# Kernel tuning notes

Measured on AMD Instinct MI355X. Metric: run time of the kernel, lower is better.

The kernel has to match this reference:

```python
import jax, jax.numpy as jnp
import numpy as np
from jax.ops import segment_sum, segment_max

N = 20000   # nodes
E = 320000  # edges (no self loops; conv adds them)
G = 64      # graphs in batch
D = 128     # embed dim
H = 64      # GATConv out channels (heads=1)
L = 6       # number of conv/mlp blocks


def setup_inputs() -> dict:
    key = jax.random.key(0)
    ks = jax.random.split(key, 24)
    x_idx = jax.random.randint(ks[0], (N,), 0, 128)
    src = jax.random.randint(ks[1], (E,), 0, N)
    dst = jax.random.randint(ks[2], (E,), 0, N)
    dst = jnp.where(src == dst, (dst + 1) % N, dst)  # remove_self_loops semantics
    edge_index = jnp.stack([src, dst])
    edge_attr_idx = jax.random.randint(ks[3], (E,), 0, 128)
    batch = (jnp.arange(N) * G) // N  # sorted graph ids, ~312 nodes/graph
    s = 0.1
    r = lambda k, shp: jax.random.normal(k, shp, dtype=jnp.float32) * s
    return {
        'x_idx': x_idx, 'edge_index': edge_index, 'edge_attr_idx': edge_attr_idx, 'batch': batch,
        'emb': r(ks[4], (128, D)),
        'conv_W': r(ks[5], (L, D, H)), 'conv_We': r(ks[6], (L, D, H)),
        'conv_att_src': r(ks[7], (L, H)), 'conv_att_dst': r(ks[8], (L, H)),
        'conv_att_edge': r(ks[9], (L, H)), 'conv_b': jnp.zeros((L, H), jnp.float32),
        'mlp_W1': r(ks[10], (L, H, H)), 'mlp_b1': jnp.zeros((L, H), jnp.float32),
        'mlp_W2': r(ks[11], (L, H, H)), 'mlp_b2': jnp.zeros((L, H), jnp.float32),
        'mlp_W3': r(ks[12], (L, H, D)), 'mlp_b3': jnp.zeros((L, D), jnp.float32),
        'g1_W1': r(ks[13], (D, H)), 'g1_b1': jnp.zeros((H,), jnp.float32),
        'g1_W2': r(ks[14], (H, 1)), 'g1_b2': jnp.zeros((1,), jnp.float32),
        'g2_W1': r(ks[15], (D, H)), 'g2_b1': jnp.zeros((H,), jnp.float32),
        'g2_W2': r(ks[16], (H, D)), 'g2_b2': jnp.zeros((D,), jnp.float32),
        'p_W1': r(ks[17], (D, H)), 'p_b1': jnp.zeros((H,), jnp.float32),
        'p_W2': r(ks[18], (H, H)), 'p_b2': jnp.zeros((H,), jnp.float32),
        'p_W3': r(ks[19], (H, 1)), 'p_b3': jnp.zeros((1,), jnp.float32),
    }


def _mlp3(x, W1, b1, W2, b2, W3, b3):
    h = jax.nn.relu(x @ W1 + b1)
    h = jax.nn.relu(h @ W2 + b2)
    return h @ W3 + b3


def reference(x_idx, edge_index, edge_attr_idx, batch, emb, conv_W, conv_We,
              conv_att_src, conv_att_dst, conv_att_edge, conv_b,
              mlp_W1, mlp_b1, mlp_W2, mlp_b2, mlp_W3, mlp_b3,
              g1_W1, g1_b1, g1_W2, g1_b2, g2_W1, g2_b1, g2_W2, g2_b2,
              p_W1, p_b1, p_W2, p_b2, p_W3, p_b3):
    n = x_idx.shape[0]
    x = emb[x_idx]                 # [N,128]
    e = emb[edge_attr_idx]         # [E,128]
    src, dst = edge_index[0], edge_index[1]
    # add_self_loops with fill_value='mean': loop attr = mean of incoming edge attrs
    deg = segment_sum(jnp.ones((e.shape[0],), x.dtype), dst, num_segments=n)
    loop_attr = segment_sum(e, dst, num_segments=n) / jnp.maximum(deg, 1.0)[:, None]
    e_full = jnp.concatenate([e, loop_attr], axis=0)             # [E+N,128]
    ar = jnp.arange(n)
    src_f = jnp.concatenate([src, ar])
    dst_f = jnp.concatenate([dst, ar])

    def gat_conv(x, i):
        h = x @ conv_W[i]                       # [N,64]
        ep = e_full @ conv_We[i]                # [E+N,64]
        a_s = h @ conv_att_src[i]               # [N]
        a_d = h @ conv_att_dst[i]               # [N]
        a_e = ep @ conv_att_edge[i]             # [E+N]
        logit = jax.nn.leaky_relu(a_s[src_f] + a_d[dst_f] + a_e, 0.2)
        m = segment_max(logit, dst_f, num_segments=n)
        w = jnp.exp(logit - m[dst_f])
        denom = segment_sum(w, dst_f, num_segments=n)
        alpha = w / denom[dst_f]
        out = segment_sum(h[src_f] * alpha[:, None], dst_f, num_segments=n)
        return out + conv_b[i]

    jkn = []
    for i in range(L):  # dropout is identity at inference
        x = gat_conv(x, i)
        x = _mlp3(x, mlp_W1[i], mlp_b1[i], mlp_W2[i], mlp_b2[i], mlp_W3[i], mlp_b3[i])
        jkn.append(x)
    jkn = jnp.stack(jkn)                                  # [6,N,128]
    ms = jnp.sqrt(jnp.sum(jnp.square(jkn), axis=2))       # [6,N]
    ni = jnp.argmax(ms, axis=0)                           # [N]
    feature = jnp.take_along_axis(jkn, ni[None, :, None], axis=0)[0]  # [N,128]

    # per-graph attention pooling (vectorized over the per-graph loop)
    h1 = (jax.nn.relu(feature @ g1_W1 + g1_b1) @ g1_W2 + g1_b2)[:, 0]  # [N]
    m = segment_max(h1, batch, num_segments=G)
    w = jnp.exp(h1 - m[batch])
    attn = w / segment_sum(w, batch, num_segments=G)[batch]            # softmax per graph
    h2 = jax.nn.relu(feature @ g2_W1 + g2_b1) @ g2_W2 + g2_b2          # [N,128]
    counts = segment_sum(jnp.ones((n,), feature.dtype), batch, num_segments=G)
    hg = segment_sum(attn[:, None] * h2, batch, num_segments=G) / counts[:, None]  # [G,128]

    out = _mlp3(hg, p_W1, p_b1, p_W2, p_b2, p_W3, p_b3)   # [G,1]
    return out[:, 0]
```

## Files before the change

### kernel.cpp

```cpp
#include <hip/hip_runtime.h>
#include <math.h>

__device__ __forceinline__ float lrelu(float x){ return x > 0.0f ? x : 0.2f*x; }
__device__ __forceinline__ float bcastf(float v, int l){
    return __int_as_float(__builtin_amdgcn_readlane(__float_as_int(v), l));
}


__global__ void k_count(const int* __restrict__ dst, int* __restrict__ cnt, int E){
    int e = blockIdx.x*256 + threadIdx.x;
    if(e < E) atomicAdd(&cnt[dst[e]], 1);
}

__global__ __launch_bounds__(1024) void k_scan(const int* __restrict__ cnt, int* __restrict__ rowptr, int n){
    __shared__ int ws[16];
    __shared__ int carrysh;
    int t = threadIdx.x, lane = t & 63, wv = t >> 6;
    if(t==0){ carrysh = 0; rowptr[0] = 0; }
    __syncthreads();
    for(int base=0; base<n; base+=1024){
        int i = base + t;
        int v = (i<n) ? cnt[i] : 0;
        int s = v;
        #pragma unroll
        for(int off=1; off<64; off<<=1){ int u = __shfl_up(s, off, 64); if(lane>=off) s += u; }
        if(lane==63) ws[wv] = s;
        __syncthreads();
        if(t < 16){
            int u = ws[t];
            #pragma unroll
            for(int off=1; off<16; off<<=1){ int u2 = __shfl_up(u, off, 16); if(t>=off) u += u2; }
            ws[t] = u;
        }
        __syncthreads();
        int carry = carrysh;
        int wbase = wv ? ws[wv-1] : 0;
        if(i<n) rowptr[i+1] = carry + wbase + s;
        int total = ws[15];
        __syncthreads();
        if(t==0) carrysh = carry + total;
        __syncthreads();
    }
}

__global__ void k_scatter(const int* __restrict__ dst, const int* __restrict__ rowptr,
                          int* __restrict__ cnt2, int* __restrict__ eid, int E){
    int e = blockIdx.x*256 + threadIdx.x;
    if(e >= E) return;
    int d = dst[e];
    int p = rowptr[d] + atomicAdd(&cnt2[d], 1);
    eid[p] = e;
}

__global__ __launch_bounds__(256) void k_sortb(const int* __restrict__ rowptr, int* __restrict__ eid, int n){
    int node = blockIdx.x*4 + (threadIdx.x>>6);
    if(node >= n) return;
    int lane = threadIdx.x & 63;
    int b = rowptr[node], e = rowptr[node+1];
    int nj = e - b;
    if(nj <= 1) return;
    if(nj <= 64){
        int v = (lane < nj) ? eid[b+lane] : 0x7fffffff;
        for(int k=2; k<=64; k<<=1){
            for(int j=k>>1; j>0; j>>=1){
                int vv = __shfl_xor(v, j, 64);
                bool up = ((lane & k) == 0);
                bool lower = ((lane & j) == 0);
                int mn = min(v,vv), mx = max(v,vv);
                v = (lower == up) ? mn : mx;
            }
        }
        if(lane < nj) eid[b+lane] = v;
    } else if(lane == 0){
        for(int i=b+1; i<e; i++){
            int key = eid[i]; int j = i-1;
            while(j>=b && eid[j] > key){ eid[j+1] = eid[j]; j--; }
            eid[j+1] = key;
        }
    }
}

__global__ __launch_bounds__(768) void k_table(const float* __restrict__ We, const float* __restrict__ atte,
                                               const float* __restrict__ emb, float* __restrict__ T){
    __shared__ float wv[768];
    int t = threadIdx.x;
    {
        int l = t>>7, k = t&127;
        const float* w = We + ((size_t)l*128 + k)*64;
        const float* a = atte + l*64;
        float s = 0.f;
        #pragma unroll 8
        for(int c=0;c<64;c++) s += w[c]*a[c];
        wv[t] = s;
    }
    __syncthreads();
    int l = t>>7, a = t&127;
    const float4* er = (const float4*)(emb + (size_t)a*128);
    const float* w = wv + l*128;
    float acc = 0.f;
    for(int k=0;k<32;k++){
        float4 v = er[k];
        acc += v.x*w[k*4+0] + v.y*w[k*4+1] + v.z*w[k*4+2] + v.w*w[k*4+3];
    }
    T[l*128 + a] = acc;
}

__global__ __launch_bounds__(256) void k_ae2(const int* __restrict__ eid, const int* __restrict__ src,
                     const int* __restrict__ eattr, const float* __restrict__ T,
                     int* __restrict__ csrsrc, float* __restrict__ ae, int E){
    __shared__ float Tl[768];
    for(int i=threadIdx.x; i<768; i+=256) Tl[i] = T[i];
    __syncthreads();
    int p = blockIdx.x*256 + threadIdx.x;
    if(p >= E) return;
    int e = eid[p];
    csrsrc[p] = src[e];
    int a = eattr[e];
    #pragma unroll
    for(int l=0;l<6;l++) ae[(size_t)l*E + p] = Tl[l*128 + a];
}


__global__ __launch_bounds__(512) void k_hx(const int* __restrict__ xidx, const float* __restrict__ emb,
        const float* __restrict__ W, const float* __restrict__ atts, const float* __restrict__ attd,
        float* __restrict__ h, float* __restrict__ as_, float* __restrict__ ad_, int n){
    __shared__ float xs[64][129];
    __shared__ float hs[64][65];
    __shared__ float redA[8][64], redB[8][64];
    int base = blockIdx.x*64;
    int t = threadIdx.x;
    {
        int r = t>>3, c0 = (t&7)*16;
        if(base + r < n){
            const float4* srcp = (const float4*)(emb + (size_t)xidx[base+r]*128 + c0);
            #pragma unroll
            for(int q=0;q<4;q++){
                float4 v = srcp[q];
                xs[r][c0+q*4+0]=v.x; xs[r][c0+q*4+1]=v.y; xs[r][c0+q*4+2]=v.z; xs[r][c0+q*4+3]=v.w;
            }
        } else {
            #pragma unroll
            for(int q=0;q<16;q++) xs[r][c0+q] = 0.f;
        }
    }
    __syncthreads();
    int lane = t & 63;
    int wid = __builtin_amdgcn_readfirstlane(t >> 6);
    int cb = wid*8;
    float acc[8] = {0,0,0,0,0,0,0,0};
    for(int k=0;k<128;k++){
        float xv = xs[lane][k];
        #pragma unroll
        for(int cc=0;cc<8;cc++) acc[cc] = fmaf(xv, W[k*64 + cb + cc], acc[cc]);
    }
    float pa=0.f, pd=0.f;
    #pragma unroll
    for(int cc=0;cc<8;cc++){
        hs[lane][cb+cc] = acc[cc];
        pa += acc[cc]*atts[cb+cc];
        pd += acc[cc]*attd[cb+cc];
    }
    redA[wid][lane]=pa; redB[wid][lane]=pd;
    __syncthreads();
    {
        int r = t>>3, c0 = (t&7)*8;
        if(base + r < n){
            float* dst = h + (size_t)(base+r)*64 + c0;
            #pragma unroll
            for(int q=0;q<8;q++) dst[q] = hs[r][c0+q];
        }
    }
    if(t < 64 && base + t < n){
        float sa=0.f, sd=0.f;
        #pragma unroll
        for(int w=0;w<8;w++){ sa += redA[w][t]; sd += redB[w][t]; }
        as_[base+t] = sa; ad_[base+t] = sd;
    }
}


__global__ __launch_bounds__(256) void k_gat(const float* __restrict__ h,
        const float* __restrict__ as_, const float* __restrict__ ad_,
        const float* __restrict__ ae, const int* __restrict__ rowptr,
        const int* __restrict__ csrsrc, const float* __restrict__ bias,
        float* __restrict__ o, int n){
    int node = blockIdx.x*4 + (threadIdx.x>>6);
    if(node >= n) return;
    int lane = threadIdx.x & 63;
    int b = rowptr[node], e = rowptr[node+1];
    float adv = ad_[node];
    float m = -1e30f, d = 0.f, sumae = 0.f;
    float a0=0.f, a1=0.f, a2=0.f, a3=0.f;
    for(int j0=b; j0<e; j0+=64){
        int nj = min(64, e-j0);
        int sj = 0; float aev = 0.f, lg = -1e30f;
        if(lane < nj){
            sj  = csrsrc[j0+lane];
            aev = ae[j0+lane];
            lg  = lrelu(as_[sj] + adv + aev);
        }
        float cm = lg, sa = aev;
        #pragma unroll
        for(int off=32; off; off>>=1){ cm = fmaxf(cm, __shfl_xor(cm,off,64)); sa += __shfl_xor(sa,off,64); }
        sumae += sa;
        float nm = fmaxf(m, cm);
        float w = (lane<nj) ? expf(lg-nm) : 0.f;
        float ws = w;
        #pragma unroll
        for(int off=32; off; off>>=1) ws += __shfl_xor(ws,off,64);
        float scale = (m > -1e29f) ? expf(m-nm) : 0.f;
        d = d*scale + ws;
        a0*=scale; a1*=scale; a2*=scale; a3*=scale;
        int j = 0;
        for(; j+3<nj; j+=4){
            a0 = fmaf(bcastf(w,j+0), h[(size_t)__builtin_amdgcn_readlane(sj,j+0)*64 + lane], a0);
            a1 = fmaf(bcastf(w,j+1), h[(size_t)__builtin_amdgcn_readlane(sj,j+1)*64 + lane], a1);
            a2 = fmaf(bcastf(w,j+2), h[(size_t)__builtin_amdgcn_readlane(sj,j+2)*64 + lane], a2);
            a3 = fmaf(bcastf(w,j+3), h[(size_t)__builtin_amdgcn_readlane(sj,j+3)*64 + lane], a3);
        }
        for(; j<nj; j++)
            a0 = fmaf(bcastf(w,j), h[(size_t)__builtin_amdgcn_readlane(sj,j)*64 + lane], a0);
        m = nm;
    }
    int deg = e - b;
    float ael = sumae / fmaxf((float)deg, 1.f);
    float ls = lrelu(as_[node] + adv + ael);
    float nm = fmaxf(m, ls);
    float scale = (m > -1e29f) ? expf(m-nm) : 0.f;
    float wl = expf(ls-nm);
    d = d*scale + wl;
    float acc = (a0+a1)+(a2+a3);
    acc = acc*scale + wl*h[(size_t)node*64 + lane];
    o[(size_t)node*64 + lane] = acc/d + bias[lane];
}


__global__ __launch_bounds__(512) void k_dense(
    const float* __restrict__ o,
    const float* __restrict__ W1, const float* __restrict__ b1,
    const float* __restrict__ W2, const float* __restrict__ b2,
    const float* __restrict__ W3, const float* __restrict__ b3,
    float* __restrict__ bestF, float* __restrict__ bestMs, int layer,
    const float* __restrict__ Wn, const float* __restrict__ atts, const float* __restrict__ attd,
    float* __restrict__ hn, float* __restrict__ asn, float* __restrict__ adn_,
    const float* __restrict__ A, const float* __restrict__ g1b1,
    const float* __restrict__ w2, const float* __restrict__ g1b2,
    const float* __restrict__ B, const float* __restrict__ g2b1,
    const float* __restrict__ C, const float* __restrict__ g2b2,
    float* __restrict__ h1, float* __restrict__ h2,
    int n, int last)
{
    __shared__ float o_s[64][65];
    __shared__ float xs[64][129];
    __shared__ float redA[8][64], redB[8][64];
    __shared__ unsigned char updf[64];
    int base = blockIdx.x*64;
    int t = threadIdx.x, lane = t & 63;
    int wid = __builtin_amdgcn_readfirstlane(t >> 6);

    {
        int r = t>>3, c0 = (t&7)*8;
        if(base + r < n){
            const float4* srcp = (const float4*)(o + (size_t)(base+r)*64 + c0);
            float4 v0 = srcp[0], v1 = srcp[1];
            o_s[r][c0+0]=v0.x; o_s[r][c0+1]=v0.y; o_s[r][c0+2]=v0.z; o_s[r][c0+3]=v0.w;
            o_s[r][c0+4]=v1.x; o_s[r][c0+5]=v1.y; o_s[r][c0+6]=v1.z; o_s[r][c0+7]=v1.w;
        } else {
            #pragma unroll
            for(int q=0;q<8;q++) o_s[r][c0+q] = 0.f;
        }
    }
    __syncthreads();

    {
        int cb = wid*8;
        float acc[8];
        #pragma unroll
        for(int cc=0;cc<8;cc++) acc[cc] = b1[cb+cc];
        for(int k=0;k<64;k++){
            float ov = o_s[lane][k];
            #pragma unroll
            for(int cc=0;cc<8;cc++) acc[cc] = fmaf(ov, W1[k*64 + cb + cc], acc[cc]);
        }
        #pragma unroll
        for(int cc=0;cc<8;cc++) xs[lane][cb+cc] = fmaxf(acc[cc], 0.f);
    }
    __syncthreads();

    {
        int cb = wid*8;
        float acc[8];
        #pragma unroll
        for(int cc=0;cc<8;cc++) acc[cc] = b2[cb+cc];
        for(int k=0;k<64;k++){
            float tv = xs[lane][k];
            #pragma unroll
            for(int cc=0;cc<8;cc++) acc[cc] = fmaf(tv, W2[k*64 + cb + cc], acc[cc]);
        }
        __syncthreads();
        #pragma unroll
        for(int cc=0;cc<8;cc++) o_s[lane][cb+cc] = fmaxf(acc[cc], 0.f);
    }
    __syncthreads();

    {
        int cb = wid*16;
        float acc[16];
        #pragma unroll
        for(int cc=0;cc<16;cc++) acc[cc] = b3[cb+cc];
        for(int k=0;k<64;k++){
            float tv = o_s[lane][k];
            #pragma unroll
            for(int cc=0;cc<16;cc++) acc[cc] = fmaf(tv, W3[k*128 + cb + cc], acc[cc]);
        }
        float ms = 0.f;
        #pragma unroll
        for(int cc=0;cc<16;cc++){ xs[lane][cb+cc] = acc[cc]; ms += acc[cc]*acc[cc]; }
        redA[wid][lane] = ms;
    }
    __syncthreads();

    if(t < 64){
        int node = base + t; bool u = false;
        if(node < n){
            float ms = 0.f;
            #pragma unroll
            for(int w=0;w<8;w++) ms += redA[w][t];
            u = (layer==0) || (ms > bestMs[node]);
            if(u) bestMs[node] = ms;
        }
        updf[t] = u ? 1 : 0;
    }
    __syncthreads();

    if(!last){
        {
            int r = t>>3, c0 = (t&7)*16;
            if(updf[r] && base + r < n){
                float* dst = bestF + (size_t)(base+r)*128 + c0;
                #pragma unroll
                for(int q=0;q<16;q++) dst[q] = xs[r][c0+q];
            }
        }
        {
            int cb = wid*8;
            float acc[8] = {0,0,0,0,0,0,0,0};
            for(int k=0;k<128;k++){
                float xv = xs[lane][k];
                #pragma unroll
                for(int cc=0;cc<8;cc++) acc[cc] = fmaf(xv, Wn[k*64 + cb + cc], acc[cc]);
            }
            float pa=0.f, pd=0.f;
            #pragma unroll
            for(int cc=0;cc<8;cc++){
                o_s[lane][cb+cc] = acc[cc];
                pa += acc[cc]*atts[cb+cc];
                pd += acc[cc]*attd[cb+cc];
            }
            redA[wid][lane]=pa; redB[wid][lane]=pd;
        }
        __syncthreads();
        {
            int r = t>>3, c0 = (t&7)*8;
            if(base + r < n){
                float* dst = hn + (size_t)(base+r)*64 + c0;
                #pragma unroll
                for(int q=0;q<8;q++) dst[q] = o_s[r][c0+q];
            }
        }
        if(t < 64 && base + t < n){
            float sa=0.f, sd=0.f;
            #pragma unroll
            for(int w=0;w<8;w++){ sa += redA[w][t]; sd += redB[w][t]; }
            asn[base+t] = sa; adn_[base+t] = sd;
        }
        return;
    }

    {
        int r = t>>3, c0 = (t&7)*16;
        if(!updf[r] && base + r < n){
            const float4* srcp = (const float4*)(bestF + (size_t)(base+r)*128 + c0);
            #pragma unroll
            for(int q=0;q<4;q++){
                float4 v = srcp[q];
                xs[r][c0+q*4+0]=v.x; xs[r][c0+q*4+1]=v.y; xs[r][c0+q*4+2]=v.z; xs[r][c0+q*4+3]=v.w;
            }
        }
    }
    __syncthreads();
    if(wid < 4){
        int cb = wid*16;
        float acc[16];
        #pragma unroll
        for(int cc=0;cc<16;cc++) acc[cc] = g1b1[cb+cc];
        for(int k=0;k<128;k++){
            float fv = xs[lane][k];
            #pragma unroll
            for(int cc=0;cc<16;cc++) acc[cc] = fmaf(fv, A[k*64 + cb + cc], acc[cc]);
        }
        float pp = 0.f;
        #pragma unroll
        for(int cc=0;cc<16;cc++) pp += fmaxf(acc[cc],0.f)*w2[cb+cc];
        redA[wid][lane] = pp;
    } else {
        int cb = (wid-4)*16;
        float acc[16];
        #pragma unroll
        for(int cc=0;cc<16;cc++) acc[cc] = g2b1[cb+cc];
        for(int k=0;k<128;k++){
            float fv = xs[lane][k];
            #pragma unroll
            for(int cc=0;cc<16;cc++) acc[cc] = fmaf(fv, B[k*64 + cb + cc], acc[cc]);
        }
        #pragma unroll
        for(int cc=0;cc<16;cc++) o_s[lane][cb+cc] = fmaxf(acc[cc],0.f);
    }
    __syncthreads();
    if(t < 64 && base + t < n)
        h1[base+t] = redA[0][t]+redA[1][t]+redA[2][t]+redA[3][t] + g1b2[0];
    {
        int cb = wid*16;
        float acc[16];
        #pragma unroll
        for(int cc=0;cc<16;cc++) acc[cc] = g2b2[cb+cc];
        for(int k=0;k<64;k++){
            float tv = o_s[lane][k];
            #pragma unroll
            for(int cc=0;cc<16;cc++) acc[cc] = fmaf(tv, C[k*128 + cb + cc], acc[cc]);
        }
        __syncthreads();
        #pragma unroll
        for(int cc=0;cc<16;cc++) xs[lane][cb+cc] = acc[cc];
    }
    __syncthreads();
    {
        int r = t>>3, c0 = (t&7)*16;
        if(base + r < n){
            float* dst = h2 + (size_t)(base+r)*128 + c0;
            #pragma unroll
            for(int q=0;q<16;q++) dst[q] = xs[r][c0+q];
        }
    }
}


__global__ __launch_bounds__(128) void k_pool2(const float* __restrict__ h1, const float* __restrict__ h2,
                      float* __restrict__ wbuf,
                      const float* __restrict__ pW1, const float* __restrict__ pb1,
                      const float* __restrict__ pW2, const float* __restrict__ pb2,
                      const float* __restrict__ pW3, const float* __restrict__ pb3,
                      float* __restrict__ out, int n, int G){
    __shared__ float sh[128];
    __shared__ float hgrow[128];
    int g = blockIdx.x, tid = threadIdx.x;
    int start = (g*n + G-1)/G, end = ((g+1)*n + G-1)/G;
    float lm = -1e30f;
    for(int i=start+tid; i<end; i+=128) lm = fmaxf(lm, h1[i]);
    sh[tid]=lm; __syncthreads();
    for(int off=64; off; off>>=1){ if(tid<off) sh[tid]=fmaxf(sh[tid],sh[tid+off]); __syncthreads(); }
    float m = sh[0]; __syncthreads();
    float lsum = 0.f;
    for(int i=start+tid; i<end; i+=128){ float w = expf(h1[i]-m); wbuf[i]=w; lsum+=w; }
    sh[tid]=lsum; __syncthreads();
    for(int off=64; off; off>>=1){ if(tid<off) sh[tid]+=sh[tid+off]; __syncthreads(); }
    float denom = sh[0];
    float a0=0.f,a1=0.f,a2=0.f,a3=0.f;
    int i = start;
    for(; i+3<end; i+=4){
        a0 = fmaf(wbuf[i+0], h2[(size_t)(i+0)*128 + tid], a0);
        a1 = fmaf(wbuf[i+1], h2[(size_t)(i+1)*128 + tid], a1);
        a2 = fmaf(wbuf[i+2], h2[(size_t)(i+2)*128 + tid], a2);
        a3 = fmaf(wbuf[i+3], h2[(size_t)(i+3)*128 + tid], a3);
    }
    for(; i<end; i++) a0 = fmaf(wbuf[i], h2[(size_t)i*128 + tid], a0);
    float acc = (a0+a1)+(a2+a3);
    hgrow[tid] = acc/denom/(float)(end-start);
    __syncthreads();
    if(tid < 64){
        float t1v = pb1[tid];
        for(int k=0;k<128;k++) t1v = fmaf(hgrow[k], pW1[k*64+tid], t1v);
        t1v = fmaxf(t1v, 0.f);
        float t2v = pb2[tid];
        for(int k=0;k<64;k++) t2v = fmaf(__shfl(t1v,k,64), pW2[k*64+tid], t2v);
        t2v = fmaxf(t2v, 0.f);
        float s = t2v * pW3[tid];
        #pragma unroll
        for(int off=32; off; off>>=1) s += __shfl_xor(s,off,64);
        if(tid==0) out[g] = s + pb3[0];
    }
}

extern "C" void kernel_launch(void* const* d_in, const int* in_sizes, int n_in,
                              void* d_out, int out_size, void* d_ws, size_t ws_size,
                              hipStream_t stream){
    const int*   x_idx   = (const int*)  d_in[0];
    const int*   eindex  = (const int*)  d_in[1];
    const int*   eattr   = (const int*)  d_in[2];
    const float* emb     = (const float*)d_in[4];
    const float* conv_W  = (const float*)d_in[5];
    const float* conv_We = (const float*)d_in[6];
    const float* att_src = (const float*)d_in[7];
    const float* att_dst = (const float*)d_in[8];
    const float* att_edg = (const float*)d_in[9];
    const float* conv_b  = (const float*)d_in[10];
    const float* mW1 = (const float*)d_in[11]; const float* mb1 = (const float*)d_in[12];
    const float* mW2 = (const float*)d_in[13]; const float* mb2 = (const float*)d_in[14];
    const float* mW3 = (const float*)d_in[15]; const float* mb3 = (const float*)d_in[16];
    const float* g1W1= (const float*)d_in[17]; const float* g1b1= (const float*)d_in[18];
    const float* g1W2= (const float*)d_in[19]; const float* g1b2= (const float*)d_in[20];
    const float* g2W1= (const float*)d_in[21]; const float* g2b1= (const float*)d_in[22];
    const float* g2W2= (const float*)d_in[23]; const float* g2b2= (const float*)d_in[24];
    const float* pW1 = (const float*)d_in[25]; const float* pb1 = (const float*)d_in[26];
    const float* pW2 = (const float*)d_in[27]; const float* pb2 = (const float*)d_in[28];
    const float* pW3 = (const float*)d_in[29]; const float* pb3 = (const float*)d_in[30];

    const int N = in_sizes[0];
    const int E = in_sizes[2];
    const int G = out_size;
    const int* src = eindex;
    const int* dst = eindex + E;
    const int NT = (N + 63) / 64;
    const int NW = (N + 3) / 4;

    char* p = (char*)d_ws;
    auto alloc = [&](size_t bytes)->void*{ void* r = (void*)p; p += (bytes + 255) & ~(size_t)255; return r; };
    float* h      = (float*)alloc((size_t)N*64*4);
    float* o      = (float*)alloc((size_t)N*64*4);
    float* bestF  = (float*)alloc((size_t)N*128*4);
    float* h2buf  = (float*)alloc((size_t)N*128*4);
    float* bestMs = (float*)alloc((size_t)N*4);
    float* as_    = (float*)alloc((size_t)N*4);
    float* ad_    = (float*)alloc((size_t)N*4);
    float* ae     = (float*)alloc((size_t)6*E*4);
    float* Tbuf   = (float*)alloc(6*128*4);
    float* h1     = (float*)alloc((size_t)N*4);
    int*   cnt    = (int*)  alloc((size_t)N*4);
    int*   cnt2   = (int*)  alloc((size_t)N*4);
    int*   rowptr = (int*)  alloc((size_t)(N+1)*4);
    int*   eid    = (int*)  alloc((size_t)E*4);
    int*   csrsrc = (int*)  alloc((size_t)E*4);

    hipMemsetAsync(cnt,  0, (size_t)N*4, stream);
    hipMemsetAsync(cnt2, 0, (size_t)N*4, stream);

    k_count<<<(E+255)/256, 256, 0, stream>>>(dst, cnt, E);
    k_scan<<<1, 1024, 0, stream>>>(cnt, rowptr, N);
    k_scatter<<<(E+255)/256, 256, 0, stream>>>(dst, rowptr, cnt2, eid, E);
    k_sortb<<<NW, 256, 0, stream>>>(rowptr, eid, N);
    k_table<<<1, 768, 0, stream>>>(conv_We, att_edg, emb, Tbuf);
    k_ae2<<<(E+255)/256, 256, 0, stream>>>(eid, src, eattr, Tbuf, csrsrc, ae, E);
    k_hx<<<NT, 512, 0, stream>>>(x_idx, emb, conv_W, att_src, att_dst, h, as_, ad_, N);

    for(int l=0; l<6; l++){
        int last = (l==5) ? 1 : 0;
        const float* Wn   = last ? conv_W  : conv_W  + (size_t)(l+1)*8192;
        const float* atsn = last ? att_src : att_src + (l+1)*64;
        const float* atdn = last ? att_dst : att_dst + (l+1)*64;
        k_gat<<<NW, 256, 0, stream>>>(h, as_, ad_, ae + (size_t)l*E, rowptr, csrsrc, conv_b + l*64, o, N);
        k_dense<<<NT, 512, 0, stream>>>(o,
            mW1 + (size_t)l*4096, mb1 + l*64, mW2 + (size_t)l*4096, mb2 + l*64,
            mW3 + (size_t)l*8192, mb3 + l*128,
            bestF, bestMs, l,
            Wn, atsn, atdn,
            h, as_, ad_,
            g1W1, g1b1, g1W2, g1b2, g2W1, g2b1, g2W2, g2b2,
            h1, h2buf,
            N, last);
    }

    k_pool2<<<G, 128, 0, stream>>>(h1, h2buf, bestMs,
            pW1, pb1, pW2, pb2, pW3, pb3, (float*)d_out, N, G);
}
```

Before: 446.6 us.

## Retile dense MLP kernel to 16 nodes per 256-thread block with float4 weights

The fused dense kernel changes from 64 nodes per 512-thread block, where each lane owned one node and one wave owned a column slice, to 16 nodes per 256-thread block. Each lane now owns one node and a group of 4 or 8 output columns, and weights are read as float4 vectors. This gives about four times as many blocks, which spreads the work across more CUs and cuts per-thread register pressure. In exchange, each block reloads every weight matrix for far fewer nodes, so weight traffic through L2 rises, and the reductions and g1/g2 branches are reorganised across 16 column groups.

```diff
diff --git a/kernel.cpp b/kernel.cpp
--- a/kernel.cpp
+++ b/kernel.cpp
@@ -235,7 +235,7 @@
 }
 
 
-__global__ __launch_bounds__(512) void k_dense(
+__global__ __launch_bounds__(256) void k_dense(
     const float* __restrict__ o,
     const float* __restrict__ W1, const float* __restrict__ b1,
     const float* __restrict__ W2, const float* __restrict__ b2,
@@ -250,84 +250,88 @@
     float* __restrict__ h1, float* __restrict__ h2,
     int n, int last)
 {
-    __shared__ float o_s[64][65];
-    __shared__ float xs[64][129];
-    __shared__ float redA[8][64], redB[8][64];
-    __shared__ unsigned char updf[64];
-    int base = blockIdx.x*64;
+    __shared__ float o_s[16][65];
+    __shared__ float xs[16][129];
+    __shared__ float redA[16][16], redB[16][16];
+    __shared__ unsigned char updf[16];
+    int base = blockIdx.x*16;
     int t = threadIdx.x, lane = t & 63;
     int wid = __builtin_amdgcn_readfirstlane(t >> 6);
-
-    {
-        int r = t>>3, c0 = (t&7)*8;
+    int node = lane & 15;
+    int q    = lane >> 4;
+    int grp  = wid*4 + q;
+    int cb4  = grp*4;
+    int cb8  = grp*8;
+
+    {
+        int r = t>>4, c0 = (t&15)*4;
         if(base + r < n){
-            const float4* srcp = (const float4*)(o + (size_t)(base+r)*64 + c0);
-            float4 v0 = srcp[0], v1 = srcp[1];
-            o_s[r][c0+0]=v0.x; o_s[r][c0+1]=v0.y; o_s[r][c0+2]=v0.z; o_s[r][c0+3]=v0.w;
-            o_s[r][c0+4]=v1.x; o_s[r][c0+5]=v1.y; o_s[r][c0+6]=v1.z; o_s[r][c0+7]=v1.w;
+            float4 v = *(const float4*)(o + (size_t)(base+r)*64 + c0);
+            o_s[r][c0+0]=v.x; o_s[r][c0+1]=v.y; o_s[r][c0+2]=v.z; o_s[r][c0+3]=v.w;
         } else {
-            #pragma unroll
-            for(int q=0;q<8;q++) o_s[r][c0+q] = 0.f;
-        }
-    }
-    __syncthreads();
-
-    {
-        int cb = wid*8;
+            o_s[r][c0+0]=0.f; o_s[r][c0+1]=0.f; o_s[r][c0+2]=0.f; o_s[r][c0+3]=0.f;
+        }
+    }
+    __syncthreads();
+
+    {
+        float acc[4];
+        #pragma unroll
+        for(int cc=0;cc<4;cc++) acc[cc] = b1[cb4+cc];
+        for(int k=0;k<64;k++){
+            float ov = o_s[node][k];
+            float4 w = *(const float4*)(W1 + k*64 + cb4);
+            acc[0]=fmaf(ov,w.x,acc[0]); acc[1]=fmaf(ov,w.y,acc[1]);
+            acc[2]=fmaf(ov,w.z,acc[2]); acc[3]=fmaf(ov,w.w,acc[3]);
+        }
+        #pragma unroll
+        for(int cc=0;cc<4;cc++) xs[node][cb4+cc] = fmaxf(acc[cc], 0.f);
+    }
+    __syncthreads();
+
+    {
+        float acc[4];
+        #pragma unroll
+        for(int cc=0;cc<4;cc++) acc[cc] = b2[cb4+cc];
+        for(int k=0;k<64;k++){
+            float tv = xs[node][k];
+            float4 w = *(const float4*)(W2 + k*64 + cb4);
+            acc[0]=fmaf(tv,w.x,acc[0]); acc[1]=fmaf(tv,w.y,acc[1]);
+            acc[2]=fmaf(tv,w.z,acc[2]); acc[3]=fmaf(tv,w.w,acc[3]);
+        }
+        #pragma unroll
+        for(int cc=0;cc<4;cc++) o_s[node][cb4+cc] = fmaxf(acc[cc], 0.f);
+    }
+    __syncthreads();
+
+    {
         float acc[8];
         #pragma unroll
-        for(int cc=0;cc<8;cc++) acc[cc] = b1[cb+cc];
+        for(int cc=0;cc<8;cc++) acc[cc] = b3[cb8+cc];
         for(int k=0;k<64;k++){
-            float ov = o_s[lane][k];
-            #pragma unroll
-            for(int cc=0;cc<8;cc++) acc[cc] = fmaf(ov, W1[k*64 + cb + cc], acc[cc]);
-        }
-        #pragma unroll
-        for(int cc=0;cc<8;cc++) xs[lane][cb+cc] = fmaxf(acc[cc], 0.f);
-    }
-    __syncthreads();
-
-    {
-        int cb = wid*8;
-        float acc[8];
-        #pragma unroll
-        for(int cc=0;cc<8;cc++) acc[cc] = b2[cb+cc];
-        for(int k=0;k<64;k++){
-            float tv = xs[lane][k];
-            #pragma unroll
-            for(int cc=0;cc<8;cc++) acc[cc] = fmaf(tv, W2[k*64 + cb + cc], acc[cc]);
-        }
-        __syncthreads();
-        #pragma unroll
-        for(int cc=0;cc<8;cc++) o_s[lane][cb+cc] = fmaxf(acc[cc], 0.f);
-    }
-    __syncthreads();
-
-    {
-        int cb = wid*16;
-        float acc[16];
-        #pragma unroll
-        for(int cc=0;cc<16;cc++) acc[cc] = b3[cb+cc];
-        for(int k=0;k<64;k++){
-            float tv = o_s[lane][k];
-            #pragma unroll
-            for(int cc=0;cc<16;cc++) acc[cc] = fmaf(tv, W3[k*128 + cb + cc], acc[cc]);
+            float tv = o_s[node][k];
+            float4 w0 = *(const float4*)(W3 + k*128 + cb8);
+            float4 w1 = *(const float4*)(W3 + k*128 + cb8 + 4);
+            acc[0]=fmaf(tv,w0.x,acc[0]); acc[1]=fmaf(tv,w0.y,acc[1]);
+            acc[2]=fmaf(tv,w0.z,acc[2]); acc[3]=fmaf(tv,w0.w,acc[3]);
+            acc[4]=fmaf(tv,w1.x,acc[4]); acc[5]=fmaf(tv,w1.y,acc[5]);
+            acc[6]=fmaf(tv,w1.z,acc[6]); acc[7]=fmaf(tv,w1.w,acc[7]);
         }
         float ms = 0.f;
         #pragma unroll
-        for(int cc=0;cc<16;cc++){ xs[lane][cb+cc] = acc[cc]; ms += acc[cc]*acc[cc]; }
-        redA[wid][lane] = ms;
-    }
-    __syncthreads();
-
-    if(t < 64){
-        int node = base + t; bool u = false;
-        if(node < n){
+        for(int cc=0;cc<8;cc++){ xs[node][cb8+cc] = acc[cc]; ms += acc[cc]*acc[cc]; }
+        redA[grp][node] = ms;
+    }
+    __syncthreads();
+
+    if(t < 16){
+        int nd = base + t; bool u = false;
+        if(nd < n){
             float ms = 0.f;
             #pragma unroll
-            for(int w=0;w<8;w++) ms += redA[w][t];
-            u = (layer==0) || (ms > bestMs[node]);
-            if(u) bestMs[node] = ms;
+            for(int g=0;g<16;g++) ms += redA[g][t];
+            u = (layer==0) || (ms > bestMs[nd]);
+            if(u) bestMs[nd] = ms;
         }
         updf[t] = u ? 1 : 0;
     }
@@ -335,111 +339,117 @@
 
     if(!last){
         {
-            int r = t>>3, c0 = (t&7)*16;
+            int r = t>>4, c0 = (t&15)*8;
             if(updf[r] && base + r < n){
                 float* dst = bestF + (size_t)(base+r)*128 + c0;
+                const float* s = &xs[r][c0];
                 #pragma unroll
-                for(int q=0;q<16;q++) dst[q] = xs[r][c0+q];
+                for(int qq=0;qq<8;qq++) dst[qq] = s[qq];
             }
         }
-        {
-            int cb = wid*8;
-            float acc[8] = {0,0,0,0,0,0,0,0};
-            for(int k=0;k<128;k++){
-                float xv = xs[lane][k];
-                #pragma unroll
-                for(int cc=0;cc<8;cc++) acc[cc] = fmaf(xv, Wn[k*64 + cb + cc], acc[cc]);
-            }
-            float pa=0.f, pd=0.f;
-            #pragma unroll
-            for(int cc=0;cc<8;cc++){
-                o_s[lane][cb+cc] = acc[cc];
-                pa += acc[cc]*atts[cb+cc];
-                pd += acc[cc]*attd[cb+cc];
-            }
-            redA[wid][lane]=pa; redB[wid][lane]=pd;
-        }
+        float acc[4] = {0,0,0,0};
+        for(int k=0;k<128;k++){
+            float xv = xs[node][k];
+            float4 w = *(const float4*)(Wn + k*64 + cb4);
+            acc[0]=fmaf(xv,w.x,acc[0]); acc[1]=fmaf(xv,w.y,acc[1]);
+            acc[2]=fmaf(xv,w.z,acc[2]); acc[3]=fmaf(xv,w.w,acc[3]);
+        }
+        float pa=0.f, pd=0.f;
+        #pragma unroll
+        for(int cc=0;cc<4;cc++){
+            pa += acc[cc]*atts[cb4+cc];
+            pd += acc[cc]*attd[cb4+cc];
+        }
+        redA[grp][node]=pa; redB[grp][node]=pd;
+        #pragma unroll
+        for(int cc=0;cc<4;cc++) o_s[node][cb4+cc] = acc[cc];
         __syncthreads();
         {
-            int r = t>>3, c0 = (t&7)*8;
+            int r = t>>4, c0 = (t&15)*4;
             if(base + r < n){
                 float* dst = hn + (size_t)(base+r)*64 + c0;
-                #pragma unroll
-                for(int q=0;q<8;q++) dst[q] = o_s[r][c0+q];
+                dst[0]=o_s[r][c0+0]; dst[1]=o_s[r][c0+1]; dst[2]=o_s[r][c0+2]; dst[3]=o_s[r][c0+3];
             }
         }
-        if(t < 64 && base + t < n){
+        if(t < 16 && base + t < n){
             float sa=0.f, sd=0.f;
             #pragma unroll
-            for(int w=0;w<8;w++){ sa += redA[w][t]; sd += redB[w][t]; }
+            for(int g=0;g<16;g++){ sa += redA[g][t]; sd += redB[g][t]; }
             asn[base+t] = sa; adn_[base+t] = sd;
         }
         return;
     }
 
     {
-        int r = t>>3, c0 = (t&7)*16;
+        int r = t>>4, c0 = (t&15)*8;
         if(!updf[r] && base + r < n){
-            const float4* srcp = (const float4*)(bestF + (size_t)(base+r)*128 + c0);
-            #pragma unroll
-            for(int q=0;q<4;q++){
-                float4 v = srcp[q];
-                xs[r][c0+q*4+0]=v.x; xs[r][c0+q*4+1]=v.y; xs[r][c0+q*4+2]=v.z; xs[r][c0+q*4+3]=v.w;
-            }
-        }
-    }
-    __syncthreads();
-    if(wid < 4){
-        int cb = wid*16;
-        float acc[16];
-        #pragma unroll
-        for(int cc=0;cc<16;cc++) acc[cc] = g1b1[cb+cc];
+            const float* s = bestF + (size_t)(base+r)*128 + c0;
+            float* d = &xs[r][c0];
+            #pragma unroll
+            for(int qq=0;qq<8;qq++) d[qq] = s[qq];
+        }
+    }
+    __syncthreads();
+    {
+        float acc[4];
+        #pragma unroll
+        for(int cc=0;cc<4;cc++) acc[cc] = g1b1[cb4+cc];
         for(int k=0;k<128;k++){
-            float fv = xs[lane][k];
-            #pragma unroll
-            for(int cc=0;cc<16;cc++) acc[cc] = fmaf(fv, A[k*64 + cb + cc], acc[cc]);
+            float fv = xs[node][k];
+            float4 w = *(const float4*)(A + k*64 + cb4);
+            acc[0]=fmaf(fv,w.x,acc[0]); acc[1]=fmaf(fv,w.y,acc[1]);
+            acc[2]=fmaf(fv,w.z,acc[2]); acc[3]=fmaf(fv,w.w,acc[3]);
         }
         float pp = 0.f;
         #pragma unroll
-        for(int cc=0;cc<16;cc++) pp += fmaxf(acc[cc],0.f)*w2[cb+cc];
-        redA[wid][lane] = pp;
-    } else {
-        int cb = (wid-4)*16;
-        float acc[16];
-        #pragma unroll
-        for(int cc=0;cc<16;cc++) acc[cc] = g2b1[cb+cc];
+        for(int cc=0;cc<4;cc++) pp += fmaxf(acc[cc],0.f)*w2[cb4+cc];
+        redA[grp][node] = pp;
+    }
+    {
+        float acc[4];
+        #pragma unroll
+        for(int cc=0;cc<4;cc++) acc[cc] = g2b1[cb4+cc];
         for(int k=0;k<128;k++){
-            float fv = xs[lane][k];
-            #pragma unroll
-            for(int cc=0;cc<16;cc++) acc[cc] = fmaf(fv, B[k*64 + cb + cc], acc[cc]);
-        }
-        #pragma unroll
-        for(int cc=0;cc<16;cc++) o_s[lane][cb+cc] = fmaxf(acc[cc],0.f);
-    }
-    __syncthreads();
-    if(t < 64 && base + t < n)
-        h1[base+t] = redA[0][t]+redA[1][t]+redA[2][t]+redA[3][t] + g1b2[0];
-    {
-        int cb = wid*16;
-        float acc[16];
-        #pragma unroll
-        for(int cc=0;cc<16;cc++) acc[cc] = g2b2[cb+cc];
+            float fv = xs[node][k];
+            float4 w = *(const float4*)(B + k*64 + cb4);
+            acc[0]=fmaf(fv,w.x,acc[0]); acc[1]=fmaf(fv,w.y,acc[1]);
+            acc[2]=fmaf(fv,w.z,acc[2]); acc[3]=fmaf(fv,w.w,acc[3]);
+        }
+        #pragma unroll
+        for(int cc=0;cc<4;cc++) o_s[node][cb4+cc] = fmaxf(acc[cc],0.f);
+    }
+    __syncthreads();
+    if(t < 16 && base + t < n){
+        float s = 0.f;
+        #pragma unroll
+        for(int g=0;g<16;g++) s += redA[g][t];
+        h1[base+t] = s + g1b2[0];
+    }
+    {
+        float acc[8];
+        #pragma unroll
+        for(int cc=0;cc<8;cc++) acc[cc] = g2b2[cb8+cc];
         for(int k=0;k<64;k++){
-            float tv = o_s[lane][k];
-            #pragma unroll
-            for(int cc=0;cc<16;cc++) acc[cc] = fmaf(tv, C[k*128 + cb + cc], acc[cc]);
+            float tv = o_s[node][k];
+            float4 w0 = *(const float4*)(C + k*128 + cb8);
+            float4 w1 = *(const float4*)(C + k*128 + cb8 + 4);
+            acc[0]=fmaf(tv,w0.x,acc[0]); acc[1]=fmaf(tv,w0.y,acc[1]);
+            acc[2]=fmaf(tv,w0.z,acc[2]); acc[3]=fmaf(tv,w0.w,acc[3]);
+            acc[4]=fmaf(tv,w1.x,acc[4]); acc[5]=fmaf(tv,w1.y,acc[5]);
+            acc[6]=fmaf(tv,w1.z,acc[6]); acc[7]=fmaf(tv,w1.w,acc[7]);
         }
         __syncthreads();
         #pragma unroll
-        for(int cc=0;cc<16;cc++) xs[lane][cb+cc] = acc[cc];
-    }
-    __syncthreads();
-    {
-        int r = t>>3, c0 = (t&7)*16;
+        for(int cc=0;cc<8;cc++) xs[node][cb8+cc] = acc[cc];
+    }
+    __syncthreads();
+    {
+        int r = t>>4, c0 = (t&15)*8;
         if(base + r < n){
             float* dst = h2 + (size_t)(base+r)*128 + c0;
-            #pragma unroll
-            for(int q=0;q<16;q++) dst[q] = xs[r][c0+q];
+            const float* s = &xs[r][c0];
+            #pragma unroll
+            for(int qq=0;qq<8;qq++) dst[qq] = s[qq];
         }
     }
 }
@@ -522,6 +532,7 @@
     const int* dst = eindex + E;
     const int NT = (N + 63) / 64;
     const int NW = (N + 3) / 4;
+    const int ND = (N + 15) / 16;
 
     char* p = (char*)d_ws;
     auto alloc = [&](size_t bytes)->void*{ void* r = (void*)p; p += (bytes + 255) & ~(size_t)255; return r; };
@@ -558,7 +569,7 @@
         const float* atsn = last ? att_src : att_src + (l+1)*64;
         const float* atdn = last ? att_dst : att_dst + (l+1)*64;
         k_gat<<<NW, 256, 0, stream>>>(h, as_, ad_, ae + (size_t)l*E, rowptr, csrsrc, conv_b + l*64, o, N);
-        k_dense<<<NT, 512, 0, stream>>>(o,
+        k_dense<<<ND, 256, 0, stream>>>(o,
             mW1 + (size_t)l*4096, mb1 + l*64, mW2 + (size_t)l*4096, mb2 + l*64,
             mW3 + (size_t)l*8192, mb3 + l*128,
             bestF, bestMs, l,
```

Result: slower. 643.3 us (+44.0%).

## Fold MLP output weights into next conv projection and precompute embedding projection

Applied to the files above, without the earlier changes.

Precomputes W3·W_next and b3·W_next per layer so the next-layer GAT projection runs as a 64-wide product on the MLP hidden state instead of a 128-wide one on the output. The first-layer projection and attention scalars are computed once per embedding vocabulary row and gathered per node. This cuts the per-node FMA work in the dense kernel and the initial projection, at the cost of a few small setup kernels and slight floating-point reassociation.

```diff
diff --git a/kernel.cpp b/kernel.cpp
--- a/kernel.cpp
+++ b/kernel.cpp
@@ -120,62 +120,74 @@
     for(int l=0;l<6;l++) ae[(size_t)l*E + p] = Tl[l*128 + a];
 }
 
-
-__global__ __launch_bounds__(512) void k_hx(const int* __restrict__ xidx, const float* __restrict__ emb,
-        const float* __restrict__ W, const float* __restrict__ atts, const float* __restrict__ attd,
-        float* __restrict__ h, float* __restrict__ as_, float* __restrict__ ad_, int n){
-    __shared__ float xs[64][129];
-    __shared__ float hs[64][65];
-    __shared__ float redA[8][64], redB[8][64];
-    int base = blockIdx.x*64;
+__global__ __launch_bounds__(256) void k_wcomb(const float* __restrict__ W3all, const float* __restrict__ Wnall,
+                                               const float* __restrict__ b3all,
+                                               float* __restrict__ Wcomb, float* __restrict__ bcomb){
+    int l = blockIdx.x;
+    const float* W3 = W3all + (size_t)l*8192;
+    const float* Wn = Wnall + (size_t)(l+1)*8192;
+    const float* b3 = b3all + l*128;
+    float* Wc = Wcomb + l*4096;
     int t = threadIdx.x;
-    {
-        int r = t>>3, c0 = (t&7)*16;
-        if(base + r < n){
-            const float4* srcp = (const float4*)(emb + (size_t)xidx[base+r]*128 + c0);
-            #pragma unroll
-            for(int q=0;q<4;q++){
-                float4 v = srcp[q];
-                xs[r][c0+q*4+0]=v.x; xs[r][c0+q*4+1]=v.y; xs[r][c0+q*4+2]=v.z; xs[r][c0+q*4+3]=v.w;
-            }
-        } else {
-            #pragma unroll
-            for(int q=0;q<16;q++) xs[r][c0+q] = 0.f;
-        }
-    }
-    __syncthreads();
-    int lane = t & 63;
-    int wid = __builtin_amdgcn_readfirstlane(t >> 6);
-    int cb = wid*8;
-    float acc[8] = {0,0,0,0,0,0,0,0};
+    for(int q=0;q<16;q++){
+        int o = t*16 + q;
+        int k = o>>6, c = o&63;
+        float s = 0.f;
+        for(int j=0;j<128;j++) s += W3[k*128+j]*Wn[j*64+c];
+        Wc[k*64+c] = s;
+    }
+    if(t < 64){
+        float s = 0.f;
+        for(int j=0;j<128;j++) s += b3[j]*Wn[j*64+t];
+        bcomb[l*64+t] = s;
+    }
+}
+
+__global__ __launch_bounds__(512) void k_hemb(const float* __restrict__ emb, const float* __restrict__ W0,
+                                              float* __restrict__ hemb){
+    int t = threadIdx.x;
+    int a = t>>2, c0 = (t&3)*16;
+    const float* er = emb + (size_t)a*128;
+    float acc[16];
+    #pragma unroll
+    for(int cc=0;cc<16;cc++) acc[cc] = 0.f;
     for(int k=0;k<128;k++){
-        float xv = xs[lane][k];
-        #pragma unroll
-        for(int cc=0;cc<8;cc++) acc[cc] = fmaf(xv, W[k*64 + cb + cc], acc[cc]);
-    }
-    float pa=0.f, pd=0.f;
+        float xv = er[k];
+        #pragma unroll
+        for(int cc=0;cc<16;cc++) acc[cc] = fmaf(xv, W0[k*64 + c0 + cc], acc[cc]);
+    }
     #pragma unroll
-    for(int cc=0;cc<8;cc++){
-        hs[lane][cb+cc] = acc[cc];
-        pa += acc[cc]*atts[cb+cc];
-        pd += acc[cc]*attd[cb+cc];
-    }
-    redA[wid][lane]=pa; redB[wid][lane]=pd;
-    __syncthreads();
-    {
-        int r = t>>3, c0 = (t&7)*8;
-        if(base + r < n){
-            float* dst = h + (size_t)(base+r)*64 + c0;
-            #pragma unroll
-            for(int q=0;q<8;q++) dst[q] = hs[r][c0+q];
-        }
-    }
-    if(t < 64 && base + t < n){
-        float sa=0.f, sd=0.f;
-        #pragma unroll
-        for(int w=0;w<8;w++){ sa += redA[w][t]; sd += redB[w][t]; }
-        as_[base+t] = sa; ad_[base+t] = sd;
-    }
+    for(int cc=0;cc<16;cc++) hemb[a*64 + c0 + cc] = acc[cc];
+}
+
+__global__ __launch_bounds__(128) void k_aemb(const float* __restrict__ hemb,
+                                              const float* __restrict__ atts, const float* __restrict__ attd,
+                                              float* __restrict__ aS, float* __restrict__ aD){
+    int a = threadIdx.x;
+    const float* hr = hemb + a*64;
+    float sa = 0.f, sd = 0.f;
+    for(int w=0;w<8;w++){
+        float pa = 0.f, pd = 0.f;
+        #pragma unroll
+        for(int cc=0;cc<8;cc++){
+            int c = w*8+cc;
+            pa += hr[c]*atts[c];
+            pd += hr[c]*attd[c];
+        }
+        sa += pa; sd += pd;
+    }
+    aS[a] = sa; aD[a] = sd;
+}
+
+__global__ void k_hx2(const int* __restrict__ xidx, const float* __restrict__ hemb,
+                      const float* __restrict__ aS, const float* __restrict__ aD,
+                      float* __restrict__ h, float* __restrict__ as_, float* __restrict__ ad_, int n){
+    int idx = blockIdx.x*256 + threadIdx.x;
+    if(idx >= n*16) return;
+    int node = idx>>4, q = idx&15, c0 = q*4;
+    int xi = xidx[node];
+    *(float4*)(h + (size_t)node*64 + c0) = *(const float4*)(hemb + (size_t)xi*64 + c0);
+    if(q==0){ as_[node] = aS[xi]; ad_[node] = aD[xi]; }
 }
 
 
@@ -241,7 +253,8 @@
     const float* __restrict__ W2, const float* __restrict__ b2,
     const float* __restrict__ W3, const float* __restrict__ b3,
     float* __restrict__ bestF, float* __restrict__ bestMs, int layer,
-    const float* __restrict__ Wn, const float* __restrict__ atts, const float* __restrict__ attd,
+    const float* __restrict__ Wc, const float* __restrict__ bc,
+    const float* __restrict__ atts, const float* __restrict__ attd,
     float* __restrict__ hn, float* __restrict__ asn, float* __restrict__ adn_,
     const float* __restrict__ A, const float* __restrict__ g1b1,
     const float* __restrict__ w2, const float* __restrict__ g1b2,
@@ -344,20 +357,24 @@
         }
         {
             int cb = wid*8;
-            float acc[8] = {0,0,0,0,0,0,0,0};
-            for(int k=0;k<128;k++){
-                float xv = xs[lane][k];
+            float acc[8];
+            #pragma unroll
+            for(int cc=0;cc<8;cc++) acc[cc] = bc[cb+cc];
+            for(int k=0;k<64;k++){
+                float tv = o_s[lane][k];
                 #pragma unroll
-                for(int cc=0;cc<8;cc++) acc[cc] = fmaf(xv, Wn[k*64 + cb + cc], acc[cc]);
+                for(int cc=0;cc<8;cc++) acc[cc] = fmaf(tv, Wc[k*64 + cb + cc], acc[cc]);
             }
             float pa=0.f, pd=0.f;
             #pragma unroll
             for(int cc=0;cc<8;cc++){
-                o_s[lane][cb+cc] = acc[cc];
                 pa += acc[cc]*atts[cb+cc];
                 pd += acc[cc]*attd[cb+cc];
             }
             redA[wid][lane]=pa; redB[wid][lane]=pd;
+            __syncthreads();
+            #pragma unroll
+            for(int cc=0;cc<8;cc++) o_s[lane][cb+cc] = acc[cc];
         }
         __syncthreads();
         {
@@ -535,6 +552,11 @@
     float* ae     = (float*)alloc((size_t)6*E*4);
     float* Tbuf   = (float*)alloc(6*128*4);
     float* h1     = (float*)alloc((size_t)N*4);
+    float* Wcomb  = (float*)alloc(5*4096*4);
+    float* bcomb  = (float*)alloc(5*64*4);
+    float* hemb   = (float*)alloc(128*64*4);
+    float* aS     = (float*)alloc(128*4);
+    float* aD     = (float*)alloc(128*4);
     int*   cnt    = (int*)  alloc((size_t)N*4);
     int*   cnt2   = (int*)  alloc((size_t)N*4);
     int*   rowptr = (int*)  alloc((size_t)(N+1)*4);
@@ -550,11 +572,15 @@
     k_sortb<<<NW, 256, 0, stream>>>(rowptr, eid, N);
     k_table<<<1, 768, 0, stream>>>(conv_We, att_edg, emb, Tbuf);
     k_ae2<<<(E+255)/256, 256, 0, stream>>>(eid, src, eattr, Tbuf, csrsrc, ae, E);
-    k_hx<<<NT, 512, 0, stream>>>(x_idx, emb, conv_W, att_src, att_dst, h, as_, ad_, N);
+    k_wcomb<<<5, 256, 0, stream>>>(mW3, conv_W, mb3, Wcomb, bcomb);
+    k_hemb<<<1, 512, 0, stream>>>(emb, conv_W, hemb);
+    k_aemb<<<1, 128, 0, stream>>>(hemb, att_src, att_dst, aS, aD);
+    k_hx2<<<(N*16+255)/256, 256, 0, stream>>>(x_idx, hemb, aS, aD, h, as_, ad_, N);
 
     for(int l=0; l<6; l++){
         int last = (l==5) ? 1 : 0;
-        const float* Wn   = last ? conv_W  : conv_W  + (size_t)(l+1)*8192;
+        const float* Wc   = last ? Wcomb : Wcomb + (size_t)l*4096;
+        const float* bcp  = last ? bcomb : bcomb + (size_t)l*64;
         const float* atsn = last ? att_src : att_src + (l+1)*64;
         const float* atdn = last ? att_dst : att_dst + (l+1)*64;
         k_gat<<<NW, 256, 0, stream>>>(h, as_, ad_, ae + (size_t)l*E, rowptr, csrsrc, conv_b + l*64, o, N);
@@ -562,7 +588,7 @@
             mW1 + (size_t)l*4096, mb1 + l*64, mW2 + (size_t)l*4096, mb2 + l*64,
             mW3 + (size_t)l*8192, mb3 + l*128,
             bestF, bestMs, l,
-            Wn, atsn, atdn,
+            Wc, bcp, atsn, atdn,
             h, as_, ad_,
             g1W1, g1b1, g1W2, g1b2, g2W1, g2b1, g2W2, g2b2,
             h1, h2buf,
```

Result: slower. 555.5 us (+24.4%).
